# Performance work log

Hardware: AMD Instinct MI355X
Metric: run time of the kernel (lower is better)

## Reference

```python
import jax, jax.numpy as jnp
import numpy as np

B, S, H = 2, 1024, 4096
NH, NKV, D = 32, 8, 128
N_REP = NH // NKV
SCALE = D ** -0.5
ROPE_BASE = 1000000.0
NEG_INF = -1e9


def _rope_tables(dtype=jnp.float32):
    inv_freq = 1.0 / (ROPE_BASE ** (jnp.arange(0, D, 2, dtype=jnp.float32) / D))
    pos = jnp.arange(S, dtype=jnp.float32)
    freqs = pos[:, None] * inv_freq[None, :]              # [S, D/2]
    emb = jnp.concatenate([freqs, freqs], axis=-1)        # [S, D]
    cos = jnp.broadcast_to(jnp.cos(emb)[None], (B, S, D)).astype(dtype)
    sin = jnp.broadcast_to(jnp.sin(emb)[None], (B, S, D)).astype(dtype)
    return cos, sin


def setup_inputs() -> dict:
    key = jax.random.key(0)
    k1, k2, k3, k4, k5 = jax.random.split(key, 5)
    hidden_states = jax.random.normal(k1, (B, S, H), dtype=jnp.float32)
    # weights stored as [in, out] so application is x @ W
    Wq = jax.random.normal(k2, (H, NH * D), dtype=jnp.float32) * (H ** -0.5)
    Wk = jax.random.normal(k3, (H, NKV * D), dtype=jnp.float32) * (H ** -0.5)
    Wv = jax.random.normal(k4, (H, NKV * D), dtype=jnp.float32) * (H ** -0.5)
    Wo = jax.random.normal(k5, (NH * D, H), dtype=jnp.float32) * ((NH * D) ** -0.5)
    cos, sin = _rope_tables()
    causal = jnp.tril(jnp.ones((S, S), dtype=bool))
    attention_mask = jnp.where(causal, 0.0, NEG_INF).astype(jnp.float32)
    attention_mask = jnp.broadcast_to(attention_mask[None, None], (B, 1, S, S))
    return {"hidden_states": hidden_states, "cos": cos, "sin": sin,
            "attention_mask": attention_mask, "Wq": Wq, "Wk": Wk, "Wv": Wv, "Wo": Wo}


def _rotate_half(x):
    x1, x2 = x[..., : D // 2], x[..., D // 2:]
    return jnp.concatenate([-x2, x1], axis=-1)


def reference(hidden_states, cos, sin, attention_mask, Wq, Wk, Wv, Wo):
    # projections -> [B, heads, S, D]
    q = (hidden_states @ Wq).reshape(B, S, NH, D).transpose(0, 2, 1, 3)
    k = (hidden_states @ Wk).reshape(B, S, NKV, D).transpose(0, 2, 1, 3)
    v = (hidden_states @ Wv).reshape(B, S, NKV, D).transpose(0, 2, 1, 3)
    # RoPE (cos/sin unsqueezed over head dim)
    c = cos[:, None, :, :]
    s = sin[:, None, :, :]
    q = q * c + _rotate_half(q) * s
    k = k * c + _rotate_half(k) * s
    # repeat_kv for GQA
    k = jnp.repeat(k, N_REP, axis=1)   # [B, NH, S, D]
    v = jnp.repeat(v, N_REP, axis=1)
    scores = jnp.einsum('bhqd,bhkd->bhqk', q, k) * SCALE + attention_mask
    weights = jax.nn.softmax(scores.astype(jnp.float32), axis=-1).astype(q.dtype)
    attn = jnp.einsum('bhqk,bhkd->bhqd', weights, v)
    attn = attn.transpose(0, 2, 1, 3).reshape(B, S, NH * D)
    return attn @ Wo
```

## Files before the change

### kernel.cpp

```cpp
#include <hip/hip_runtime.h>

typedef unsigned short u16;
typedef __bf16 bf16x8 __attribute__((ext_vector_type(8)));
typedef float f32x4 __attribute__((ext_vector_type(4)));

#define SCALE_QK 0.08838834764831845f
#define LOG2E 1.4426950408889634f
#define NEGBIG (-1e9f)

static __device__ __forceinline__ float bf2f(u16 u) {
  union { float f; unsigned int i; } x; x.i = ((unsigned int)u) << 16; return x.f;
}
static __device__ __forceinline__ u16 f2bf(float f) {
  union { float f; unsigned int i; } x; x.f = f;
  return (u16)((x.i + 0x7fffu + ((x.i >> 16) & 1u)) >> 16);
}
static __device__ __forceinline__ void async16(const u16* g, u16* s) {
  __builtin_amdgcn_global_load_lds(
      (const __attribute__((address_space(1))) void*)g,
      (__attribute__((address_space(3))) void*)s, 16, 0, 0);
}

__global__ __launch_bounds__(64) void detect_dtype(
    const void* p0, const void* p1, const void* p2, const void* p3,
    const void* p4, const void* p5, int* flags) {
  const void* ps[6] = {p0, p1, p2, p3, p4, p5};
  const u16* p = (const u16*)ps[blockIdx.x];
  int lane = threadIdx.x;
  u16 u = p[2 * lane];
  int e = (u >> 7) & 0xFF;
  int plaus = (e >= 112 && e <= 143) ? 1 : 0;
  unsigned long long m = __ballot(plaus);
  if (lane == 0) {
    flags[blockIdx.x] = (__popcll(m) < 32) ? 1 : 0;
    if (blockIdx.x == 0) flags[6] = 0;
  }
}

static __device__ __forceinline__ void transpose_body(
    const void* __restrict__ src, u16* __restrict__ dst, int N, int K,
    int n0, int k0, int f32in, u16* t) {
  const int LT = 74;
  const int tid = threadIdx.x;
  for (int c = tid; c < 512; c += 256) {
    int r = c >> 3, ch = (c & 7) * 8;
    u16* tp = t + r * LT + ch;
    if (f32in) {
      const float* p = (const float*)src + (size_t)(k0 + r) * N + n0 + ch;
      float4 v0 = *(const float4*)p;
      float4 v1 = *(const float4*)(p + 4);
      tp[0] = f2bf(v0.x); tp[1] = f2bf(v0.y); tp[2] = f2bf(v0.z); tp[3] = f2bf(v0.w);
      tp[4] = f2bf(v1.x); tp[5] = f2bf(v1.y); tp[6] = f2bf(v1.z); tp[7] = f2bf(v1.w);
    } else {
      uint4 v = *(const uint4*)((const u16*)src + (size_t)(k0 + r) * N + n0 + ch);
      const u16* pv = (const u16*)&v;
#pragma unroll
      for (int e = 0; e < 8; ++e) tp[e] = pv[e];
    }
  }
  __syncthreads();
  for (int c = tid; c < 512; c += 256) {
    int rr = c >> 3, cc = (c & 7) * 8;
    u16 tmp[8];
#pragma unroll
    for (int e = 0; e < 8; ++e) tmp[e] = t[(cc + e) * LT + rr];
    *(uint4*)(dst + (size_t)(n0 + rr) * K + k0 + cc) = *(const uint4*)tmp;
  }
}

__global__ __launch_bounds__(256) void transpose_to_bf16(
    const void* __restrict__ src, u16* __restrict__ dst, int N, int K,
    const int* __restrict__ flag) {
  __shared__ u16 t[64 * 74];
  transpose_body(src, dst, N, K, blockIdx.x * 64, blockIdx.y * 64, *flag, t);
}

__global__ __launch_bounds__(256) void transpose_qkv(
    const void* __restrict__ Wq, const void* __restrict__ Wk,
    const void* __restrict__ Wv, u16* __restrict__ dst,
    const int* __restrict__ flags) {
  __shared__ u16 t[64 * 74];
  int bx = blockIdx.x;
  const void* src; u16* d; int N; int f32in; int nx;
  if (bx < 64)      { src = Wq; d = dst;                         N = 4096; f32in = flags[2]; nx = bx; }
  else if (bx < 80) { src = Wk; d = dst + (size_t)4096 * 4096;   N = 1024; f32in = flags[3]; nx = bx - 64; }
  else              { src = Wv; d = dst + (size_t)5120 * 4096;   N = 1024; f32in = flags[4]; nx = bx - 80; }
  transpose_body(src, d, N, 4096, nx * 64, blockIdx.y * 64, f32in, t);
}

__global__ __launch_bounds__(256) void cast_to_bf16(
    const void* __restrict__ src, u16* __restrict__ dst, const int* __restrict__ flag) {
  int i = (blockIdx.x * 256 + threadIdx.x) * 8;
  if (*flag) {
    float4 v0 = *(const float4*)((const float*)src + i);
    float4 v1 = *(const float4*)((const float*)src + i + 4);
    u16 tmp[8] = {f2bf(v0.x), f2bf(v0.y), f2bf(v0.z), f2bf(v0.w),
                  f2bf(v1.x), f2bf(v1.y), f2bf(v1.z), f2bf(v1.w)};
    *(uint4*)(dst + i) = *(const uint4*)tmp;
  } else {
    *(uint4*)(dst + i) = *(const uint4*)((const u16*)src + i);
  }
}

__global__ __launch_bounds__(256, 2) void gemm_bt(
    const u16* __restrict__ A, const u16* __restrict__ Bt, void* __restrict__ C,
    int K, int lda, int ldb, int ldc, const int* __restrict__ oflag) {
  __shared__ u16 sA[128 * 32];
  __shared__ u16 sB[128 * 32];
  const int tid = threadIdx.x;
  const int wave = tid >> 6, lane = tid & 63;
  const int quad = lane >> 4, l16 = lane & 15;
  const int wr = wave >> 1, wc = wave & 1;
  const int bm = blockIdx.y << 7, bn = blockIdx.x << 7;
  const int f32out = *oflag;

  f32x4 acc[4][4] = {};

  const int c0 = tid, c1 = tid + 256;
  const int r0 = c0 >> 2, h0 = (c0 & 3) * 8;
  const int r1 = c1 >> 2, h1 = (c1 & 3) * 8;
  const u16* a0 = A + (size_t)(bm + r0) * lda + h0;
  const u16* a1 = A + (size_t)(bm + r1) * lda + h1;
  const u16* b0 = Bt + (size_t)(bn + r0) * ldb + h0;
  const u16* b1 = Bt + (size_t)(bn + r1) * ldb + h1;

  for (int k0 = 0; k0 < K; k0 += 32) {
    async16(a0 + k0, sA + c0 * 8);
    async16(a1 + k0, sA + c1 * 8);
    async16(b0 + k0, sB + c0 * 8);
    async16(b1 + k0, sB + c1 * 8);
    __syncthreads();
    bf16x8 af[4], bv[4];
#pragma unroll
    for (int i = 0; i < 4; ++i)
      af[i] = *(const bf16x8*)(sA + (wr * 64 + i * 16 + l16) * 32 + quad * 8);
#pragma unroll
    for (int j = 0; j < 4; ++j)
      bv[j] = *(const bf16x8*)(sB + (wc * 64 + j * 16 + l16) * 32 + quad * 8);
#pragma unroll
    for (int i = 0; i < 4; ++i)
#pragma unroll
      for (int j = 0; j < 4; ++j)
        acc[i][j] =
            __builtin_amdgcn_mfma_f32_16x16x32_bf16(af[i], bv[j], acc[i][j], 0, 0, 0);
    __syncthreads();
  }
#pragma unroll
  for (int i = 0; i < 4; ++i) {
    int row = bm + wr * 64 + i * 16 + quad * 4;
#pragma unroll
    for (int j = 0; j < 4; ++j) {
      int col = bn + wc * 64 + j * 16 + l16;
#pragma unroll
      for (int r = 0; r < 4; ++r) {
        size_t idx = (size_t)(row + r) * ldc + col;
        if (f32out) ((float*)C)[idx] = acc[i][j][r];
        else ((u16*)C)[idx] = f2bf(acc[i][j][r]);
      }
    }
  }
}

__global__ __launch_bounds__(256) void rope_kernel(
    u16* __restrict__ QKV, const void* __restrict__ cosb,
    const void* __restrict__ sinb, const int* __restrict__ flag) {
  int idx = blockIdx.x * 256 + threadIdx.x;
  int d8 = (idx & 7) * 8;
  int rest = idx >> 3;
  int slot = rest % 40;
  int tok = rest / 40;
  int col = (slot < 32) ? (slot * 128 + d8) : (4096 + (slot - 32) * 128 + d8);
  size_t base = (size_t)tok * 6144 + col;
  uint4 va = *(const uint4*)(QKV + base);
  uint4 vb = *(const uint4*)(QKV + base + 64);
  const u16* pa = (const u16*)&va;
  const u16* pb = (const u16*)&vb;
  size_t cb = (size_t)tok * 128 + d8;
  float c1[8], s1[8], c2[8], s2[8];
  if (*flag) {
    const float* cp = (const float*)cosb + cb;
    const float* sp = (const float*)sinb + cb;
    float4 t0 = *(const float4*)cp,        t1 = *(const float4*)(cp + 4);
    float4 t2 = *(const float4*)(cp + 64), t3 = *(const float4*)(cp + 68);
    float4 u0 = *(const float4*)sp,        u1 = *(const float4*)(sp + 4);
    float4 u2 = *(const float4*)(sp + 64), u3 = *(const float4*)(sp + 68);
    const float* tf = (const float*)&t0;
    (void)tf;
    c1[0]=t0.x;c1[1]=t0.y;c1[2]=t0.z;c1[3]=t0.w;c1[4]=t1.x;c1[5]=t1.y;c1[6]=t1.z;c1[7]=t1.w;
    c2[0]=t2.x;c2[1]=t2.y;c2[2]=t2.z;c2[3]=t2.w;c2[4]=t3.x;c2[5]=t3.y;c2[6]=t3.z;c2[7]=t3.w;
    s1[0]=u0.x;s1[1]=u0.y;s1[2]=u0.z;s1[3]=u0.w;s1[4]=u1.x;s1[5]=u1.y;s1[6]=u1.z;s1[7]=u1.w;
    s2[0]=u2.x;s2[1]=u2.y;s2[2]=u2.z;s2[3]=u2.w;s2[4]=u3.x;s2[5]=u3.y;s2[6]=u3.z;s2[7]=u3.w;
  } else {
    const u16* cp = (const u16*)cosb + cb;
    const u16* sp = (const u16*)sinb + cb;
    uint4 t0 = *(const uint4*)cp, t1 = *(const uint4*)(cp + 64);
    uint4 u0 = *(const uint4*)sp, u1 = *(const uint4*)(sp + 64);
    const u16* q0 = (const u16*)&t0; const u16* q1 = (const u16*)&t1;
    const u16* r0 = (const u16*)&u0; const u16* r1 = (const u16*)&u1;
#pragma unroll
    for (int e = 0; e < 8; ++e) {
      c1[e] = bf2f(q0[e]); c2[e] = bf2f(q1[e]);
      s1[e] = bf2f(r0[e]); s2[e] = bf2f(r1[e]);
    }
  }
  u16 o1[8], o2[8];
#pragma unroll
  for (int e = 0; e < 8; ++e) {
    float x1 = bf2f(pa[e]), x2 = bf2f(pb[e]);
    o1[e] = f2bf(x1 * c1[e] - x2 * s1[e]);
    o2[e] = f2bf(x2 * c2[e] + x1 * s2[e]);
  }
  *(uint4*)(QKV + base) = *(const uint4*)o1;
  *(uint4*)(QKV + base + 64) = *(const uint4*)o2;
}

__global__ __launch_bounds__(256, 3) void attn_kernel(
    const u16* __restrict__ QKV, u16* __restrict__ O) {
  const int LK = 136;
  const int LP = 72;
  __shared__ u16 sK[64 * LK];
  __shared__ u16 sV[128 * 64];
  __shared__ u16 sP[64 * LP];
  const int tid = threadIdx.x, wave = tid >> 6, lane = tid & 63;
  const int quad = lane >> 4, l16 = lane & 15;
  const int pp = blockIdx.x, h = blockIdx.y, b = blockIdx.z;
  const int kvh = h >> 2;
  const size_t tb = (size_t)b * 1024 * 6144;
  const u16* Qg = QKV + tb + (size_t)h * 128;
  const u16* Kg = QKV + tb + 4096 + (size_t)kvh * 128;
  const u16* Vg = QKV + tb + 5120 + (size_t)kvh * 128;

#pragma unroll 1
  for (int pass = 0; pass < 2; ++pass) {
    const int qt = pass ? (15 - pp) : pp;

    bf16x8 qa[4];
    {
      const int qrow = qt * 64 + wave * 16 + l16;
#pragma unroll
      for (int kc = 0; kc < 4; ++kc) {
        bf16x8 v = *(const bf16x8*)(Qg + (size_t)qrow * 6144 + kc * 32 + quad * 8);
#pragma unroll
        for (int e = 0; e < 8; ++e) v[e] = (__bf16)((float)v[e] * (SCALE_QK * LOG2E));
        qa[kc] = v;
      }
    }

    uint4 kreg[4], vreg[4];
#pragma unroll
    for (int i = 0; i < 4; ++i) {
      int c = i * 256 + tid, row = c >> 4, ch = (c & 15) * 8;
      kreg[i] = *(const uint4*)(Kg + (size_t)row * 6144 + ch);
      vreg[i] = *(const uint4*)(Vg + (size_t)row * 6144 + ch);
    }

    float m_run = -INFINITY, l_run = 0.f;
    f32x4 oacc[8] = {};
    const int qg = qt * 64 + wave * 16 + l16;

    const int nkb = qt + 1;
    for (int kb = 0; kb < nkb; ++kb) {
#pragma unroll
      for (int i = 0; i < 4; ++i) {
        int c = i * 256 + tid, row = c >> 4, ch = (c & 15) * 8;
        *(uint4*)(sK + row * LK + ch) = kreg[i];
        const u16* pw = (const u16*)&vreg[i];
#pragma unroll
        for (int e = 0; e < 8; ++e) {
          int d = ch + e;
          sV[d * 64 + ((((row >> 3) ^ (d >> 3)) & 7) << 3) + (row & 7)] = pw[e];
        }
      }
      __syncthreads();
      if (kb + 1 < nkb) {
#pragma unroll
        for (int i = 0; i < 4; ++i) {
          int c = i * 256 + tid, row = c >> 4, ch = (c & 15) * 8;
          kreg[i] = *(const uint4*)(Kg + (size_t)((kb + 1) * 64 + row) * 6144 + ch);
          vreg[i] = *(const uint4*)(Vg + (size_t)((kb + 1) * 64 + row) * 6144 + ch);
        }
      }

      f32x4 st[4] = {};
#pragma unroll
      for (int kc = 0; kc < 4; ++kc)
#pragma unroll
        for (int j = 0; j < 4; ++j) {
          bf16x8 bb = *(const bf16x8*)(sK + (j * 16 + l16) * LK + kc * 32 + quad * 8);
          st[j] = __builtin_amdgcn_mfma_f32_16x16x32_bf16(bb, qa[kc], st[j], 0, 0, 0);
        }

      const int kg0 = kb * 64 + quad * 4;
      float mloc = NEGBIG;
#pragma unroll
      for (int j = 0; j < 4; ++j)
#pragma unroll
        for (int r = 0; r < 4; ++r) {
          float v = st[j][r];
          if (kg0 + j * 16 + r > qg) v = NEGBIG;
          st[j][r] = v;
          mloc = fmaxf(mloc, v);
        }
      mloc = fmaxf(mloc, __shfl_xor(mloc, 16, 64));
      mloc = fmaxf(mloc, __shfl_xor(mloc, 32, 64));

      if (__any(mloc - m_run > 8.0f)) {
        float mn = fmaxf(m_run, mloc);
        float alpha = exp2f(m_run - mn);
        m_run = mn;
        l_run *= alpha;
        float ar[4];
#pragma unroll
        for (int r = 0; r < 4; ++r) ar[r] = __shfl(alpha, quad * 4 + r, 64);
#pragma unroll
        for (int dt = 0; dt < 8; ++dt)
#pragma unroll
          for (int r = 0; r < 4; ++r) oacc[dt][r] *= ar[r];
      }

      float lad = 0.f;
#pragma unroll
      for (int j = 0; j < 4; ++j)
#pragma unroll
        for (int r = 0; r < 4; ++r) {
          float p = exp2f(st[j][r] - m_run);
          st[j][r] = p;
          lad += p;
        }
      lad += __shfl_xor(lad, 16, 64);
      lad += __shfl_xor(lad, 32, 64);
      l_run += lad;

#pragma unroll
      for (int j = 0; j < 4; ++j)
#pragma unroll
        for (int r = 0; r < 4; ++r)
          sP[(wave * 16 + l16) * LP + j * 16 + quad * 4 + r] = f2bf(st[j][r]);
      __asm__ __volatile__("s_waitcnt lgkmcnt(0)" ::: "memory");

#pragma unroll
      for (int kc = 0; kc < 2; ++kc) {
        bf16x8 a = *(const bf16x8*)(sP + (wave * 16 + l16) * LP + kc * 32 + quad * 8);
#pragma unroll
        for (int dt = 0; dt < 8; ++dt) {
          int d = dt * 16 + l16;
          int chk = ((kc * 4 + quad) ^ (d >> 3)) & 7;
          bf16x8 bb = *(const bf16x8*)(sV + d * 64 + chk * 8);
          oacc[dt] = __builtin_amdgcn_mfma_f32_16x16x32_bf16(a, bb, oacc[dt], 0, 0, 0);
        }
      }
      __syncthreads();
    }

    float lfin[4];
#pragma unroll
    for (int r = 0; r < 4; ++r) lfin[r] = __shfl(l_run, quad * 4 + r, 64);

    const int srow = qt * 64 + wave * 16 + quad * 4;
#pragma unroll
    for (int dt = 0; dt < 8; ++dt)
#pragma unroll
      for (int r = 0; r < 4; ++r) {
        float val = oacc[dt][r] / lfin[r];
        O[((size_t)b * 1024 + srow + r) * 4096 + h * 128 + dt * 16 + l16] = f2bf(val);
      }
  }
}

extern "C" void kernel_launch(void* const* d_in, const int* in_sizes, int n_in,
                              void* d_out, int out_size, void* d_ws, size_t ws_size,
                              hipStream_t stream) {
  (void)in_sizes; (void)n_in; (void)out_size; (void)ws_size;
  const void* hidden = d_in[0];
  const void* cosb   = d_in[1];
  const void* sinb   = d_in[2];
  const void* Wq = d_in[4];
  const void* Wk = d_in[5];
  const void* Wv = d_in[6];
  const void* Wo = d_in[7];

  u16* ws = (u16*)d_ws;
  u16* Wqkvt = ws;
  u16* Wot   = ws;
  u16* Xb    = ws + (size_t)25165824;
  u16* attnb = Xb;
  u16* QKV   = ws + (size_t)33554432;
  int* flags = (int*)(ws + (size_t)46137344);

  detect_dtype<<<6, 64, 0, stream>>>(hidden, cosb, Wq, Wk, Wv, Wo, flags);

  transpose_qkv<<<dim3(96, 64), 256, 0, stream>>>(Wq, Wk, Wv, Wqkvt, flags);
  cast_to_bf16<<<4096, 256, 0, stream>>>(hidden, Xb, flags + 0);

  gemm_bt<<<dim3(48, 16), 256, 0, stream>>>(Xb, Wqkvt, QKV, 4096, 4096, 4096, 6144, flags + 6);
  rope_kernel<<<2560, 256, 0, stream>>>(QKV, cosb, sinb, flags + 1);

  transpose_to_bf16<<<dim3(64, 64), 256, 0, stream>>>(Wo, Wot, 4096, 4096, flags + 5);

  attn_kernel<<<dim3(8, 32, 2), 256, 0, stream>>>(QKV, attnb);
  gemm_bt<<<dim3(32, 16), 256, 0, stream>>>(attnb, Wot, d_out, 4096, 4096, 4096, 4096, flags + 0);
}
```

Before: 502.7 us.

## Replace GEMM with double-buffered, phased 256-tile kernel using swizzled LDS

Replaces the 128x128, BK=32 single-buffer GEMM with a templated 512-thread kernel that uses 256x256 or 256x128 tiles, BK=64, and double-buffered LDS. Global-to-LDS loads for the next K tile are spread across four compute phases. It also adds XOR-swizzled LDS columns to avoid bank conflicts, a grid remap to improve L2 locality, and s_setprio around the MFMA bursts. The aim is to hide memory latency and cut synchronisation and LDS overhead in the QKV and output projections, at the cost of heavier register and LDS use that may reduce occupancy.

```diff
diff --git a/kernel.cpp b/kernel.cpp
--- a/kernel.cpp
+++ b/kernel.cpp
@@ -102,60 +102,118 @@
   }
 }
 
-__global__ __launch_bounds__(256, 2) void gemm_bt(
+template <int BM, int BN, int NWM, int NWN>
+__global__ __launch_bounds__(512, 2) void gemm_ph(
     const u16* __restrict__ A, const u16* __restrict__ Bt, void* __restrict__ C,
     int K, int lda, int ldb, int ldc, const int* __restrict__ oflag) {
-  __shared__ u16 sA[128 * 32];
-  __shared__ u16 sB[128 * 32];
+  constexpr int LA = BM / 64, LB = BN / 64, L = LA + LB;
+  constexpr int WM = BM / NWM, WN = BN / NWN;
+  constexpr int FM = WM / 16, FN = WN / 16;
+  constexpr int BUF = (BM + BN) * 64;
+  __shared__ u16 lds[BUF * 2];
   const int tid = threadIdx.x;
   const int wave = tid >> 6, lane = tid & 63;
   const int quad = lane >> 4, l16 = lane & 15;
-  const int wr = wave >> 1, wc = wave & 1;
-  const int bm = blockIdx.y << 7, bn = blockIdx.x << 7;
+  const int wr = wave / NWN, wc = wave % NWN;
+
+  const int nwg = gridDim.x * gridDim.y;
+  const int flat = blockIdx.y * gridDim.x + blockIdx.x;
+  const int swz = (flat & 7) * (nwg >> 3) + (flat >> 3);
+  const int bm = (swz / gridDim.x) * BM;
+  const int bn = (swz % gridDim.x) * BN;
   const int f32out = *oflag;
 
-  f32x4 acc[4][4] = {};
-
-  const int c0 = tid, c1 = tid + 256;
-  const int r0 = c0 >> 2, h0 = (c0 & 3) * 8;
-  const int r1 = c1 >> 2, h1 = (c1 & 3) * 8;
-  const u16* a0 = A + (size_t)(bm + r0) * lda + h0;
-  const u16* a1 = A + (size_t)(bm + r1) * lda + h1;
-  const u16* b0 = Bt + (size_t)(bn + r0) * ldb + h0;
-  const u16* b1 = Bt + (size_t)(bn + r1) * ldb + h1;
-
-  for (int k0 = 0; k0 < K; k0 += 32) {
-    async16(a0 + k0, sA + c0 * 8);
-    async16(a1 + k0, sA + c1 * 8);
-    async16(b0 + k0, sB + c0 * 8);
-    async16(b1 + k0, sB + c1 * 8);
-    __syncthreads();
-    bf16x8 af[4], bv[4];
-#pragma unroll
-    for (int i = 0; i < 4; ++i)
-      af[i] = *(const bf16x8*)(sA + (wr * 64 + i * 16 + l16) * 32 + quad * 8);
-#pragma unroll
-    for (int j = 0; j < 4; ++j)
-      bv[j] = *(const bf16x8*)(sB + (wc * 64 + j * 16 + l16) * 32 + quad * 8);
-#pragma unroll
-    for (int i = 0; i < 4; ++i)
-#pragma unroll
-      for (int j = 0; j < 4; ++j)
-        acc[i][j] =
-            __builtin_amdgcn_mfma_f32_16x16x32_bf16(af[i], bv[j], acc[i][j], 0, 0, 0);
-    __syncthreads();
-  }
-#pragma unroll
-  for (int i = 0; i < 4; ++i) {
-    int row = bm + wr * 64 + i * 16 + quad * 4;
-#pragma unroll
-    for (int j = 0; j < 4; ++j) {
-      int col = bn + wc * 64 + j * 16 + l16;
+  const int srow = tid >> 3;
+  const int scol = ((tid & 7) ^ (srow & 7)) * 8;
+  const u16* gA = A + (size_t)(bm + srow) * lda + scol;
+  const u16* gB = Bt + (size_t)(bn + srow) * ldb + scol;
+
+  f32x4 acc[FM][FN] = {};
+  const int nk = K >> 6;
+
+#pragma unroll
+  for (int i = 0; i < LA; ++i)
+    async16(gA + (size_t)(i * 64) * lda, lds + i * 4096 + tid * 8);
+#pragma unroll
+  for (int j = 0; j < LB; ++j)
+    async16(gB + (size_t)(j * 64) * ldb, lds + BM * 64 + j * 4096 + tid * 8);
+  __asm__ __volatile__("s_waitcnt vmcnt(0)" ::: "memory");
+  __asm__ __volatile__("s_barrier" ::: "memory");
+
+  const int ch0 = (quad ^ (l16 & 7)) * 8;
+  const int ch1 = ((4 + quad) ^ (l16 & 7)) * 8;
+
+  for (int t = 0; t < nk; ++t) {
+    const u16* bufA = lds + (t & 1) * BUF;
+    const u16* bufB = bufA + BM * 64;
+    u16* nbuf = lds + ((t + 1) & 1) * BUF;
+    const int kn = (t + 1) << 6;
+    const bool more = (t + 1) < nk;
+
+    bf16x8 af[FM / 2][2];
+    bf16x8 bv[FN][2];
+#pragma unroll
+    for (int ph = 0; ph < 4; ++ph) {
+      const int mh = ph >> 1, nh = ph & 1;
+      if (ph == 0 || ph == 2) {
+#pragma unroll
+        for (int mi = 0; mi < FM / 2; ++mi) {
+          const u16* p = bufA + (wr * WM + (mh * (FM / 2) + mi) * 16 + l16) * 64;
+          af[mi][0] = *(const bf16x8*)(p + ch0);
+          af[mi][1] = *(const bf16x8*)(p + ch1);
+        }
+      }
+      if (ph < 2) {
+#pragma unroll
+        for (int ni = 0; ni < FN / 2; ++ni) {
+          const int n = ph * (FN / 2) + ni;
+          const u16* p = bufB + (wc * WN + n * 16 + l16) * 64;
+          bv[n][0] = *(const bf16x8*)(p + ch0);
+          bv[n][1] = *(const bf16x8*)(p + ch1);
+        }
+      }
+      if (more) {
+#pragma unroll
+        for (int i = 0; i < LA; ++i)
+          if (i >= ph * L / 4 && i < (ph + 1) * L / 4)
+            async16(gA + (size_t)(i * 64) * lda + kn, nbuf + i * 4096 + tid * 8);
+#pragma unroll
+        for (int j = 0; j < LB; ++j)
+          if (LA + j >= ph * L / 4 && LA + j < (ph + 1) * L / 4)
+            async16(gB + (size_t)(j * 64) * ldb + kn,
+                    nbuf + BM * 64 + j * 4096 + tid * 8);
+      }
+      __asm__ __volatile__("s_barrier" ::: "memory");
+      __asm__ __volatile__("s_waitcnt lgkmcnt(0)" ::: "memory");
+      __builtin_amdgcn_sched_barrier(0);
+      __builtin_amdgcn_s_setprio(1);
+#pragma unroll
+      for (int mi = 0; mi < FM / 2; ++mi)
+#pragma unroll
+        for (int ni = 0; ni < FN / 2; ++ni) {
+          const int cm = mh * (FM / 2) + mi, cn = nh * (FN / 2) + ni;
+          acc[cm][cn] = __builtin_amdgcn_mfma_f32_16x16x32_bf16(
+              af[mi][0], bv[cn][0], acc[cm][cn], 0, 0, 0);
+          acc[cm][cn] = __builtin_amdgcn_mfma_f32_16x16x32_bf16(
+              af[mi][1], bv[cn][1], acc[cm][cn], 0, 0, 0);
+        }
+      __builtin_amdgcn_s_setprio(0);
+      if (ph == 3) __asm__ __volatile__("s_waitcnt vmcnt(0)" ::: "memory");
+      __asm__ __volatile__("s_barrier" ::: "memory");
+    }
+  }
+
+#pragma unroll
+  for (int mi = 0; mi < FM; ++mi) {
+    int row = bm + wr * WM + mi * 16 + quad * 4;
+#pragma unroll
+    for (int ni = 0; ni < FN; ++ni) {
+      int col = bn + wc * WN + ni * 16 + l16;
 #pragma unroll
       for (int r = 0; r < 4; ++r) {
         size_t idx = (size_t)(row + r) * ldc + col;
-        if (f32out) ((float*)C)[idx] = acc[i][j][r];
-        else ((u16*)C)[idx] = f2bf(acc[i][j][r]);
+        if (f32out) ((float*)C)[idx] = acc[mi][ni][r];
+        else ((u16*)C)[idx] = f2bf(acc[mi][ni][r]);
       }
     }
   }
@@ -184,8 +242,6 @@
     float4 t2 = *(const float4*)(cp + 64), t3 = *(const float4*)(cp + 68);
     float4 u0 = *(const float4*)sp,        u1 = *(const float4*)(sp + 4);
     float4 u2 = *(const float4*)(sp + 64), u3 = *(const float4*)(sp + 68);
-    const float* tf = (const float*)&t0;
-    (void)tf;
     c1[0]=t0.x;c1[1]=t0.y;c1[2]=t0.z;c1[3]=t0.w;c1[4]=t1.x;c1[5]=t1.y;c1[6]=t1.z;c1[7]=t1.w;
     c2[0]=t2.x;c2[1]=t2.y;c2[2]=t2.z;c2[3]=t2.w;c2[4]=t3.x;c2[5]=t3.y;c2[6]=t3.z;c2[7]=t3.w;
     s1[0]=u0.x;s1[1]=u0.y;s1[2]=u0.z;s1[3]=u0.w;s1[4]=u1.x;s1[5]=u1.y;s1[6]=u1.z;s1[7]=u1.w;
@@ -392,11 +448,14 @@
   transpose_qkv<<<dim3(96, 64), 256, 0, stream>>>(Wq, Wk, Wv, Wqkvt, flags);
   cast_to_bf16<<<4096, 256, 0, stream>>>(hidden, Xb, flags + 0);
 
-  gemm_bt<<<dim3(48, 16), 256, 0, stream>>>(Xb, Wqkvt, QKV, 4096, 4096, 4096, 6144, flags + 6);
+  gemm_ph<256, 256, 2, 4><<<dim3(24, 8), 512, 0, stream>>>(
+      Xb, Wqkvt, QKV, 4096, 4096, 4096, 6144, flags + 6);
   rope_kernel<<<2560, 256, 0, stream>>>(QKV, cosb, sinb, flags + 1);
 
   transpose_to_bf16<<<dim3(64, 64), 256, 0, stream>>>(Wo, Wot, 4096, 4096, flags + 5);
 
   attn_kernel<<<dim3(8, 32, 2), 256, 0, stream>>>(QKV, attnb);
-  gemm_bt<<<dim3(32, 16), 256, 0, stream>>>(attnb, Wot, d_out, 4096, 4096, 4096, 4096, flags + 0);
-}
+
+  gemm_ph<256, 128, 4, 2><<<dim3(32, 8), 512, 0, stream>>>(
+      attnb, Wot, d_out, 4096, 4096, 4096, 4096, flags + 0);
+}
```

After: 505.8 us. No clear change (+0.6%).
